# Optimization experiments

Hardware: AMD Instinct MI355X
Metric: run time of the kernel (lower is better)

The kernel has to match this reference:

```python
import jax, jax.numpy as jnp
import numpy as np
import math

H = 1024
E = 8
K = 2
CF = 1.5
THR = 0.5


def setup_inputs() -> dict:
    key = jax.random.key(0)
    ks = jax.random.split(key, 8)
    s = 0.02
    return {
        'hidden_states': jax.random.normal(ks[0], (2, 2048, H), jnp.float32),
        # importance predictor: Linear(H, H//2) -> ReLU -> Linear(H//2, 1) -> Sigmoid
        'wi1': jax.random.normal(ks[1], (H, H // 2), jnp.float32) * s,
        'bi1': jnp.zeros((H // 2,), jnp.float32),
        'wi2': jax.random.normal(ks[2], (H // 2, 1), jnp.float32) * s,
        'bi2': jnp.zeros((1,), jnp.float32),
        # router_important: Linear(H,H) -> ReLU -> Linear(H,E)
        'wr1': jax.random.normal(ks[3], (H, H), jnp.float32) * s,
        'br1': jnp.zeros((H,), jnp.float32),
        'wr2': jax.random.normal(ks[4], (H, E), jnp.float32) * s,
        'br2': jnp.zeros((E,), jnp.float32),
        # router_unimportant: Linear(H,H) -> ReLU -> Linear(H,E)
        'wu1': jax.random.normal(ks[5], (H, H), jnp.float32) * s,
        'bu1': jnp.zeros((H,), jnp.float32),
        'wu2': jax.random.normal(ks[6], (H, E), jnp.float32) * s,
        'bu2': jnp.zeros((E,), jnp.float32),
    }


def reference(hidden_states, wi1, bi1, wi2, bi2, wr1, br1, wr2, br2, wu1, bu1, wu2, bu2):
    x = hidden_states
    B, S, _ = x.shape
    N = B * S
    capacity = int(B * S * CF * K / E)  # static per-expert capacity

    # dual-gate routing
    importance = jax.nn.sigmoid(jnp.maximum(x @ wi1 + bi1, 0.0) @ wi2 + bi2)  # [B,S,1]
    imp_mask = (importance > THR).astype(x.dtype)                              # [B,S,1]
    logits_imp = jnp.maximum(x @ wr1 + br1, 0.0) @ wr2 + br2                   # [B,S,E]
    logits_unimp = jnp.maximum(x @ wu1 + bu1, 0.0) @ wu2 + bu2                 # [B,S,E]
    router_logits = imp_mask * logits_imp + (1.0 - imp_mask) * logits_unimp
    router_probs = jax.nn.softmax(router_logits, axis=-1)                      # [B,S,E]

    top_k_probs, top_k_indices = jax.lax.top_k(router_probs, K)
    top_k_probs = top_k_probs / top_k_probs.sum(-1, keepdims=True)

    # capacity-constrained dispatch: k-major assignment order (outer loop over k,
    # tokens in order), position within expert = running count, drop if >= capacity
    ef = top_k_indices.reshape(N, K).T.reshape(-1)   # [K*N] expert id, k-major
    pf = top_k_probs.reshape(N, K).T.reshape(-1)     # [K*N] gate prob
    tf = jnp.tile(jnp.arange(N), K)                  # [K*N] token id
    oh = jax.nn.one_hot(ef, E, dtype=jnp.int32)      # [K*N, E]
    pos = jnp.take_along_axis(jnp.cumsum(oh, axis=0), ef[:, None], 1)[:, 0] - 1
    keep = pos < capacity
    posc = jnp.clip(pos, 0, capacity - 1)

    zeros = jnp.zeros((N, E, capacity), x.dtype)
    dispatch = zeros.at[tf, ef, posc].add(keep.astype(x.dtype))
    combine = zeros.at[tf, ef, posc].add(jnp.where(keep, pf, 0.0))
    dispatch = dispatch.reshape(B, S, E, capacity)
    combine = combine.reshape(B, S, E, capacity)

    # aux losses
    rppe = router_probs.mean((0, 1))
    entropy_loss = jnp.sum(rppe * jnp.log(rppe * E + 1e-9))
    imp_sum = (router_probs * imp_mask).sum((0, 1)) + 1e-9
    ippe = imp_sum / imp_sum.sum()
    imp_entropy = -jnp.sum(ippe * jnp.log(ippe + 1e-9))
    aux_loss = entropy_loss - 0.1 * (imp_entropy / math.log(E))

    return dispatch, combine, router_probs, aux_loss, importance
```

## Files before the change

### kernel.cpp

```cpp
#include <hip/hip_runtime.h>
#include <math.h>

#define HDIM  1024
#define HHALF 512
#define NEXP  8
#define NTOK  4096
#define CAP   1536
#define NTOT  2560
#define TOTAL_DC (2u * NTOK * NEXP * CAP)

typedef _Float16 f16x8 __attribute__((ext_vector_type(8)));
typedef float    f32x4 __attribute__((ext_vector_type(4)));

#define GEMM_BLOCKS 640
#define FILL_BLOCKS 1408
#define S_LO 2048.0f
#define S_W  32.0f

__global__ __launch_bounds__(256) void prep(
    const float* __restrict__ x,
    const float* __restrict__ wi1, const float* __restrict__ wr1,
    const float* __restrict__ wu1,
    const float* __restrict__ bi1, const float* __restrict__ br1,
    const float* __restrict__ bu1,
    _Float16* __restrict__ Ah, _Float16* __restrict__ Al,
    _Float16* __restrict__ Bth, _Float16* __restrict__ Btl,
    float* __restrict__ bias_cat)
{
    __shared__ float tile[64][65];
    const int bid = blockIdx.x, tid = threadIdx.x;

    if (bid < 2048) {
        const int i8 = bid * 256 + tid;
        const float4* x4 = (const float4*)x;
        float4 v0 = x4[i8 * 2];
        float4 v1 = x4[i8 * 2 + 1];
        float f[8] = {v0.x, v0.y, v0.z, v0.w, v1.x, v1.y, v1.z, v1.w};
        f16x8 hi, lo;
#pragma unroll
        for (int j = 0; j < 8; j++) {
            _Float16 h = (_Float16)f[j];
            hi[j] = h;
            lo[j] = (_Float16)((f[j] - (float)h) * S_LO);
        }
        *(f16x8*)&Ah[(size_t)i8 * 8] = hi;
        *(f16x8*)&Al[(size_t)i8 * 8] = lo;
        return;
    }
    if (bid < 2688) {
        int local; const float* src; int C, nof;
        int b = bid - 2048;
        if (b < 128)      { src = wi1; C = 512;  nof = 0;    local = b; }
        else if (b < 384) { src = wr1; C = 1024; nof = 512;  local = b - 128; }
        else              { src = wu1; C = 1024; nof = 1536; local = b - 384; }
        const int nti = local >> 4, kti = local & 15;
#pragma unroll
        for (int p = 0; p < 16; p++) {
            int e = p * 256 + tid;
            int kr = e >> 6, nc = e & 63;
            tile[kr][nc] = src[(size_t)(kti * 64 + kr) * C + nti * 64 + nc];
        }
        __syncthreads();
#pragma unroll
        for (int p = 0; p < 16; p++) {
            int e = p * 256 + tid;
            int nl = e >> 6, kk = e & 63;
            float w32 = tile[kk][nl] * S_W;
            _Float16 h = (_Float16)w32;
            _Float16 l = (_Float16)((w32 - (float)h) * S_LO);
            const size_t o = (size_t)(nof + nti * 64 + nl) * 1024 + kti * 64 + kk;
            Bth[o] = h;
            Btl[o] = l;
        }
        return;
    }
    for (int i = tid; i < NTOT; i += 256) {
        float v = (i < 512) ? bi1[i] : (i < 1536) ? br1[i - 512] : bu1[i - 1536];
        bias_cat[i] = v;
    }
}

__global__ __launch_bounds__(256, 2) void gemm_fill(
    const _Float16* __restrict__ Ah, const _Float16* __restrict__ Al,
    const _Float16* __restrict__ Bth, const _Float16* __restrict__ Btl,
    const float* __restrict__ bias_cat, float* __restrict__ H,
    float* __restrict__ out)
{
    if (blockIdx.x >= GEMM_BLOCKS) {
        f32x4* o4 = (f32x4*)out;
        const unsigned total4 = TOTAL_DC / 4;
        unsigned i = (blockIdx.x - GEMM_BLOCKS) * 256u + threadIdx.x;
        const unsigned stride = FILL_BLOCKS * 256u;
        const f32x4 z = {0.f, 0.f, 0.f, 0.f};
        for (; i < total4; i += stride)
            __builtin_nontemporal_store(z, o4 + i);
        return;
    }

    __shared__ _Float16 lds[2][4][128][32];

    const int tid = threadIdx.x;
    const int lane = tid & 63, wid = tid >> 6;

    const int xcd = blockIdx.x & 7;
    const int idx = blockIdx.x >> 3;
    const int bm  = xcd * 4 + (idx & 3);
    const int bn  = idx >> 2;
    const int rowBase = bm * 128, colBase = bn * 128;

    const _Float16* gb =
        (wid == 0) ? Ah  + (size_t)rowBase * 1024 :
        (wid == 1) ? Al  + (size_t)rowBase * 1024 :
        (wid == 2) ? Bth + (size_t)colBase * 1024 :
                     Btl + (size_t)colBase * 1024;
    const int lrow = lane >> 2;
    const int lkg  = lane & 3;

    f32x4 acc_hh[4][4], acc_x[4][4];
    const f32x4 z4 = {0.f, 0.f, 0.f, 0.f};
#pragma unroll
    for (int i = 0; i < 4; i++)
#pragma unroll
        for (int j = 0; j < 4; j++) { acc_hh[i][j] = z4; acc_x[i][j] = z4; }

    const int mw = (wid >> 1) * 64, nw = (wid & 1) * 64;
    const int fr = lane & 15, s = lane >> 4;

#define STAGE(buf, k0)                                                        \
    {                                                                         \
        _Pragma("unroll")                                                     \
        for (int i = 0; i < 8; i++) {                                         \
            const int r = i * 16 + lrow;                                      \
            __builtin_amdgcn_global_load_lds(                                 \
                (const void*)(gb + (size_t)r * 1024 + (k0) + lkg * 8),        \
                (void*)&lds[buf][wid][i * 16][0], 16, 0, 0);                  \
        }                                                                     \
    }

#define COMPUTE(buf)                                                          \
    {                                                                         \
        f16x8 fa_h[4], fa_l[4], fb_h[4], fb_l[4];                             \
        _Pragma("unroll")                                                     \
        for (int mf = 0; mf < 4; mf++) {                                      \
            fa_h[mf] = *(const f16x8*)&lds[buf][0][mw + mf * 16 + fr][s * 8]; \
            fa_l[mf] = *(const f16x8*)&lds[buf][1][mw + mf * 16 + fr][s * 8]; \
        }                                                                     \
        _Pragma("unroll")                                                     \
        for (int nf = 0; nf < 4; nf++) {                                      \
            fb_h[nf] = *(const f16x8*)&lds[buf][2][nw + nf * 16 + fr][s * 8]; \
            fb_l[nf] = *(const f16x8*)&lds[buf][3][nw + nf * 16 + fr][s * 8]; \
        }                                                                     \
        _Pragma("unroll")                                                     \
        for (int mf = 0; mf < 4; mf++)                                        \
            _Pragma("unroll")                                                 \
            for (int nf = 0; nf < 4; nf++) {                                  \
                acc_hh[mf][nf] = __builtin_amdgcn_mfma_f32_16x16x32_f16(      \
                    fa_h[mf], fb_h[nf], acc_hh[mf][nf], 0, 0, 0);             \
                acc_x[mf][nf] = __builtin_amdgcn_mfma_f32_16x16x32_f16(       \
                    fa_h[mf], fb_l[nf], acc_x[mf][nf], 0, 0, 0);              \
                acc_x[mf][nf] = __builtin_amdgcn_mfma_f32_16x16x32_f16(       \
                    fa_l[mf], fb_h[nf], acc_x[mf][nf], 0, 0, 0);              \
            }                                                                 \
    }

    STAGE(0, 0);
    __syncthreads();

    for (int t = 0; t < 32; t += 2) {
        if (t + 1 < 32) STAGE(1, (t + 1) * 32);
        COMPUTE(0);
        __syncthreads();
        if (t + 2 < 32) STAGE(0, (t + 2) * 32);
        COMPUTE(1);
        __syncthreads();
    }
#undef STAGE
#undef COMPUTE

#pragma unroll
    for (int mf = 0; mf < 4; mf++) {
        const int row0 = rowBase + mw + mf * 16 + (lane >> 4) * 4;
#pragma unroll
        for (int nf = 0; nf < 4; nf++) {
            const int col = colBase + nw + nf * 16 + (lane & 15);
            const float b = bias_cat[col];
#pragma unroll
            for (int r = 0; r < 4; r++) {
                float v = (acc_hh[mf][nf][r] + acc_x[mf][nf][r] * (1.0f / S_LO))
                          * (1.0f / S_W) + b;
                H[(size_t)(row0 + r) * NTOT + col] = fmaxf(v, 0.f);
            }
        }
    }
}

__global__ __launch_bounds__(256) void second_layer(
    const float* __restrict__ H,
    const float* __restrict__ wi2, const float* __restrict__ bi2,
    const float* __restrict__ wr2, const float* __restrict__ br2,
    const float* __restrict__ wu2, const float* __restrict__ bu2,
    float* __restrict__ oprobs, float* __restrict__ oimp,
    int* __restrict__ tke, float* __restrict__ tkp)
{
    const int t = blockIdx.x;
    const int tid = threadIdx.x;
    const float* hrow = H + (size_t)t * NTOT;

    float pi = 0.f;
    float pr[8], pu[8];
#pragma unroll
    for (int e = 0; e < 8; e++) { pr[e] = 0.f; pu[e] = 0.f; }

    for (int j = tid; j < HHALF; j += 256) pi = fmaf(hrow[j], wi2[j], pi);
    for (int j = tid; j < HDIM; j += 256) {
        float a = hrow[512 + j], b = hrow[1536 + j];
#pragma unroll
        for (int e = 0; e < 8; e++) {
            pr[e] = fmaf(a, wr2[j * 8 + e], pr[e]);
            pu[e] = fmaf(b, wu2[j * 8 + e], pu[e]);
        }
    }

#pragma unroll
    for (int off = 32; off > 0; off >>= 1) {
        pi += __shfl_down(pi, off, 64);
#pragma unroll
        for (int e = 0; e < 8; e++) {
            pr[e] += __shfl_down(pr[e], off, 64);
            pu[e] += __shfl_down(pu[e], off, 64);
        }
    }

    __shared__ float red[4][17];
    const int lane = tid & 63, wv = tid >> 6;
    if (lane == 0) {
        red[wv][0] = pi;
#pragma unroll
        for (int e = 0; e < 8; e++) { red[wv][1 + e] = pr[e]; red[wv][9 + e] = pu[e]; }
    }
    __syncthreads();

    if (tid == 0) {
        float si = red[0][0] + red[1][0] + red[2][0] + red[3][0] + bi2[0];
        float sig = 1.f / (1.f + expf(-si));
        oimp[t] = sig;
        const bool m = sig > 0.5f;
        float lg[8];
#pragma unroll
        for (int e = 0; e < 8; e++) {
            float vr = red[0][1 + e] + red[1][1 + e] + red[2][1 + e] + red[3][1 + e] + br2[e];
            float vu = red[0][9 + e] + red[1][9 + e] + red[2][9 + e] + red[3][9 + e] + bu2[e];
            lg[e] = m ? vr : vu;
        }
        float mx = lg[0];
#pragma unroll
        for (int e = 1; e < 8; e++) mx = fmaxf(mx, lg[e]);
        float p[8], sum = 0.f;
#pragma unroll
        for (int e = 0; e < 8; e++) { p[e] = expf(lg[e] - mx); sum += p[e]; }
        const float inv = 1.f / sum;
#pragma unroll
        for (int e = 0; e < 8; e++) { p[e] *= inv; oprobs[t * 8 + e] = p[e]; }
        int i1 = 0;
#pragma unroll
        for (int e = 1; e < 8; e++) if (p[e] > p[i1]) i1 = e;
        int i2 = (i1 == 0) ? 1 : 0;
#pragma unroll
        for (int e = 0; e < 8; e++) if (e != i1 && p[e] > p[i2]) i2 = e;
        const float ps = p[i1] + p[i2];
        tke[t]        = i1;
        tke[NTOK + t] = i2;
        tkp[t]        = p[i1] / ps;
        tkp[NTOK + t] = p[i2] / ps;
    }
}

__global__ __launch_bounds__(256) void aux_kernel(
    const float* __restrict__ oprobs, const float* __restrict__ oimp,
    float* __restrict__ oaux)
{
    const int tid = threadIdx.x;
    float ap[8], ai[8];
#pragma unroll
    for (int e = 0; e < 8; e++) { ap[e] = 0.f; ai[e] = 0.f; }

    for (int t = tid; t < NTOK; t += 256) {
        const float msk = (oimp[t] > 0.5f) ? 1.f : 0.f;
#pragma unroll
        for (int e = 0; e < 8; e++) {
            float p = oprobs[t * 8 + e];
            ap[e] += p;
            ai[e] = fmaf(msk, p, ai[e]);
        }
    }
#pragma unroll
    for (int off = 32; off > 0; off >>= 1) {
#pragma unroll
        for (int e = 0; e < 8; e++) {
            ap[e] += __shfl_down(ap[e], off, 64);
            ai[e] += __shfl_down(ai[e], off, 64);
        }
    }
    __shared__ float red[4][16];
    const int lane = tid & 63, wv = tid >> 6;
    if (lane == 0) {
#pragma unroll
        for (int e = 0; e < 8; e++) { red[wv][e] = ap[e]; red[wv][8 + e] = ai[e]; }
    }
    __syncthreads();
    if (tid == 0) {
        float ent = 0.f, tot = 0.f, isv[8];
#pragma unroll
        for (int e = 0; e < 8; e++) {
            float sp = red[0][e] + red[1][e] + red[2][e] + red[3][e];
            float sm = red[0][8 + e] + red[1][8 + e] + red[2][8 + e] + red[3][8 + e];
            float r = sp / (float)NTOK;
            ent += r * logf(r * 8.f + 1e-9f);
            isv[e] = sm + 1e-9f;
            tot += isv[e];
        }
        float ie = 0.f;
#pragma unroll
        for (int e = 0; e < 8; e++) {
            float q = isv[e] / tot;
            ie -= q * logf(q + 1e-9f);
        }
        oaux[0] = ent - 0.1f * (ie / logf(8.f));
    }
}

__global__ __launch_bounds__(256) void scan_scatter(
    const int* __restrict__ tke, const float* __restrict__ tkp,
    float* __restrict__ out)
{
    __shared__ unsigned char se[2 * NTOK];
    __shared__ float         sp[2 * NTOK];
    __shared__ int cnts[256][8];

    const int tid = threadIdx.x;

    for (int i = tid; i < 2 * NTOK; i += 256) {
        se[i] = (unsigned char)tke[i];
        sp[i] = tkp[i];
    }
    __syncthreads();

    const int base = tid * 32;
    int c[8];
#pragma unroll
    for (int e = 0; e < 8; e++) c[e] = 0;
    for (int i = 0; i < 32; i++) {
        int e = se[base + i];
#pragma unroll
        for (int k = 0; k < 8; k++) c[k] += (e == k) ? 1 : 0;
    }
#pragma unroll
    for (int e = 0; e < 8; e++) cnts[tid][e] = c[e];
    __syncthreads();

    if (tid < 8) {
        int run = 0;
        for (int i = 0; i < 256; i++) {
            int v = cnts[i][tid];
            cnts[i][tid] = run;
            run += v;
        }
    }
    __syncthreads();

    int basecnt[8];
#pragma unroll
    for (int e = 0; e < 8; e++) basecnt[e] = cnts[tid][e];

    float* comb = out + (size_t)NTOK * NEXP * CAP;

    for (int i = 0; i < 32; i++) {
        const int idx = base + i;
        const int e = se[idx];
        int pos = 0;
#pragma unroll
        for (int k = 0; k < 8; k++)
            if (e == k) { pos = basecnt[k]; basecnt[k]++; }
        if (pos < CAP) {
            const int tok = idx & (NTOK - 1);
            const size_t o = ((size_t)tok * NEXP + e) * CAP + pos;
            out[o]  = 1.0f;
            comb[o] = sp[idx];
        }
    }
}

__global__ __launch_bounds__(256) void gemm_bias_relu(
    const float* __restrict__ A, const float* __restrict__ B,
    const float* __restrict__ bias, float* __restrict__ Hout, int N)
{
    __shared__ float As[16][132];
    __shared__ float Bs[16][132];
    const int tid = threadIdx.x;
    const int tx = tid & 15, ty = tid >> 4;
    const int rowBase = blockIdx.y * 128, colBase = blockIdx.x * 128;
    const int lrow = tid >> 1, lkq = (tid & 1) * 8;
    const int bkk = tid >> 4, bcol = (tid & 15) * 8;
    float acc[8][8];
#pragma unroll
    for (int i = 0; i < 8; i++)
#pragma unroll
        for (int j = 0; j < 8; j++) acc[i][j] = 0.f;
    const float* Aptr = A + (size_t)(rowBase + lrow) * HDIM + lkq;
    const float* Bptr = B + (size_t)bkk * N + colBase + bcol;
    for (int k0 = 0; k0 < HDIM; k0 += 16) {
        float4 a0 = *(const float4*)(Aptr + k0);
        float4 a1 = *(const float4*)(Aptr + k0 + 4);
        float4 b0 = *(const float4*)(Bptr + (size_t)k0 * N);
        float4 b1 = *(const float4*)(Bptr + (size_t)k0 * N + 4);
        __syncthreads();
        As[lkq + 0][lrow] = a0.x; As[lkq + 1][lrow] = a0.y;
        As[lkq + 2][lrow] = a0.z; As[lkq + 3][lrow] = a0.w;
        As[lkq + 4][lrow] = a1.x; As[lkq + 5][lrow] = a1.y;
        As[lkq + 6][lrow] = a1.z; As[lkq + 7][lrow] = a1.w;
        *(float4*)&Bs[bkk][bcol] = b0;
        *(float4*)&Bs[bkk][bcol + 4] = b1;
        __syncthreads();
#pragma unroll
        for (int kk = 0; kk < 16; kk++) {
            float4 x0 = *(const float4*)&As[kk][ty * 8];
            float4 x1 = *(const float4*)&As[kk][ty * 8 + 4];
            float4 y0 = *(const float4*)&Bs[kk][tx * 8];
            float4 y1 = *(const float4*)&Bs[kk][tx * 8 + 4];
            float av[8] = {x0.x, x0.y, x0.z, x0.w, x1.x, x1.y, x1.z, x1.w};
            float bv[8] = {y0.x, y0.y, y0.z, y0.w, y1.x, y1.y, y1.z, y1.w};
#pragma unroll
            for (int i = 0; i < 8; i++)
#pragma unroll
                for (int j = 0; j < 8; j++)
                    acc[i][j] = fmaf(av[i], bv[j], acc[i][j]);
        }
    }
#pragma unroll
    for (int i = 0; i < 8; i++) {
        const int r = rowBase + ty * 8 + i, c = colBase + tx * 8;
#pragma unroll
        for (int j = 0; j < 8; j += 4) {
            float4 v;
            v.x = fmaxf(acc[i][j + 0] + bias[c + j + 0], 0.f);
            v.y = fmaxf(acc[i][j + 1] + bias[c + j + 1], 0.f);
            v.z = fmaxf(acc[i][j + 2] + bias[c + j + 2], 0.f);
            v.w = fmaxf(acc[i][j + 3] + bias[c + j + 3], 0.f);
            *(float4*)&Hout[(size_t)r * N + c + j] = v;
        }
    }
}

__global__ __launch_bounds__(256) void zerofill_fb(float* __restrict__ out)
{
    f32x4* o4 = (f32x4*)out;
    const unsigned total4 = TOTAL_DC / 4;
    unsigned i = blockIdx.x * 256u + threadIdx.x;
    const unsigned stride = gridDim.x * 256u;
    const f32x4 z = {0.f, 0.f, 0.f, 0.f};
    for (; i < total4; i += stride) o4[i] = z;
}

__global__ __launch_bounds__(256) void second_layer_sep(
    const float* __restrict__ h_i, const float* __restrict__ h_r,
    const float* __restrict__ h_u,
    const float* __restrict__ wi2, const float* __restrict__ bi2,
    const float* __restrict__ wr2, const float* __restrict__ br2,
    const float* __restrict__ wu2, const float* __restrict__ bu2,
    float* __restrict__ oprobs, float* __restrict__ oimp,
    int* __restrict__ tke, float* __restrict__ tkp)
{
    const int t = blockIdx.x;
    const int tid = threadIdx.x;
    float pi = 0.f;
    float pr[8], pu[8];
#pragma unroll
    for (int e = 0; e < 8; e++) { pr[e] = 0.f; pu[e] = 0.f; }
    const float* hi = h_i + (size_t)t * HHALF;
    const float* hr = h_r + (size_t)t * HDIM;
    const float* hu = h_u + (size_t)t * HDIM;
    for (int j = tid; j < HHALF; j += 256) pi = fmaf(hi[j], wi2[j], pi);
    for (int j = tid; j < HDIM; j += 256) {
        float a = hr[j], b = hu[j];
#pragma unroll
        for (int e = 0; e < 8; e++) {
            pr[e] = fmaf(a, wr2[j * 8 + e], pr[e]);
            pu[e] = fmaf(b, wu2[j * 8 + e], pu[e]);
        }
    }
#pragma unroll
    for (int off = 32; off > 0; off >>= 1) {
        pi += __shfl_down(pi, off, 64);
#pragma unroll
        for (int e = 0; e < 8; e++) {
            pr[e] += __shfl_down(pr[e], off, 64);
            pu[e] += __shfl_down(pu[e], off, 64);
        }
    }
    __shared__ float red[4][17];
    const int lane = tid & 63, wv = tid >> 6;
    if (lane == 0) {
        red[wv][0] = pi;
#pragma unroll
        for (int e = 0; e < 8; e++) { red[wv][1 + e] = pr[e]; red[wv][9 + e] = pu[e]; }
    }
    __syncthreads();
    if (tid == 0) {
        float si = red[0][0] + red[1][0] + red[2][0] + red[3][0] + bi2[0];
        float sig = 1.f / (1.f + expf(-si));
        oimp[t] = sig;
        const bool m = sig > 0.5f;
        float lg[8];
#pragma unroll
        for (int e = 0; e < 8; e++) {
            float vr = red[0][1 + e] + red[1][1 + e] + red[2][1 + e] + red[3][1 + e] + br2[e];
            float vu = red[0][9 + e] + red[1][9 + e] + red[2][9 + e] + red[3][9 + e] + bu2[e];
            lg[e] = m ? vr : vu;
        }
        float mx = lg[0];
#pragma unroll
        for (int e = 1; e < 8; e++) mx = fmaxf(mx, lg[e]);
        float p[8], s = 0.f;
#pragma unroll
        for (int e = 0; e < 8; e++) { p[e] = expf(lg[e] - mx); s += p[e]; }
        const float inv = 1.f / s;
#pragma unroll
        for (int e = 0; e < 8; e++) { p[e] *= inv; oprobs[t * 8 + e] = p[e]; }
        int i1 = 0;
#pragma unroll
        for (int e = 1; e < 8; e++) if (p[e] > p[i1]) i1 = e;
        int i2 = (i1 == 0) ? 1 : 0;
#pragma unroll
        for (int e = 0; e < 8; e++) if (e != i1 && p[e] > p[i2]) i2 = e;
        const float ps = p[i1] + p[i2];
        tke[t]        = i1;
        tke[NTOK + t] = i2;
        tkp[t]        = p[i1] / ps;
        tkp[NTOK + t] = p[i2] / ps;
    }
}

extern "C" void kernel_launch(void* const* d_in, const int* in_sizes, int n_in,
                              void* d_out, int out_size, void* d_ws, size_t ws_size,
                              hipStream_t stream) {
    const float* x   = (const float*)d_in[0];
    const float* wi1 = (const float*)d_in[1];
    const float* bi1 = (const float*)d_in[2];
    const float* wi2 = (const float*)d_in[3];
    const float* bi2 = (const float*)d_in[4];
    const float* wr1 = (const float*)d_in[5];
    const float* br1 = (const float*)d_in[6];
    const float* wr2 = (const float*)d_in[7];
    const float* br2 = (const float*)d_in[8];
    const float* wu1 = (const float*)d_in[9];
    const float* bu1 = (const float*)d_in[10];
    const float* wu2 = (const float*)d_in[11];
    const float* bu2 = (const float*)d_in[12];

    float* out    = (float*)d_out;
    float* oprobs = out + (size_t)TOTAL_DC;
    float* oaux   = oprobs + NTOK * NEXP;
    float* oimp   = oaux + 1;

    const size_t szH  = (size_t)NTOK * NTOT * 4;
    const size_t szA  = (size_t)NTOK * HDIM * 2;
    const size_t szB  = (size_t)NTOT * HDIM * 2;
    const size_t need = szH + 2 * szA + 2 * szB + NTOT * 4
                      + 2 * NTOK * 4 + 2 * NTOK * 4 + 4096;
    dim3 blk(256);

    if (ws_size >= need) {
        char* p = (char*)d_ws;
        float*    H    = (float*)p;            p += szH;
        _Float16* Ah   = (_Float16*)p;         p += szA;
        _Float16* Al   = (_Float16*)p;         p += szA;
        _Float16* Bth  = (_Float16*)p;         p += szB;
        _Float16* Btl  = (_Float16*)p;         p += szB;
        float*    bias = (float*)p;            p += NTOT * 4;
        int*      tke  = (int*)p;              p += 2 * NTOK * 4;
        float*    tkp  = (float*)p;

        prep<<<2689, blk, 0, stream>>>(x, wi1, wr1, wu1, bi1, br1, bu1,
                                       Ah, Al, Bth, Btl, bias);
        gemm_fill<<<GEMM_BLOCKS + FILL_BLOCKS, blk, 0, stream>>>(
            Ah, Al, Bth, Btl, bias, H, out);
        second_layer<<<NTOK, blk, 0, stream>>>(H, wi2, bi2, wr2, br2, wu2, bu2,
                                               oprobs, oimp, tke, tkp);
        aux_kernel<<<1, blk, 0, stream>>>(oprobs, oimp, oaux);
        scan_scatter<<<1, blk, 0, stream>>>(tke, tkp, out);
    } else {
        float* h_i = out;
        float* h_r = h_i + (size_t)NTOK * HHALF;
        float* h_u = h_r + (size_t)NTOK * HDIM;
        int*   tke  = (int*)d_ws;
        float* tkp  = (float*)d_ws + 2 * NTOK;

        gemm_bias_relu<<<dim3(HHALF / 128, NTOK / 128), blk, 0, stream>>>(x, wi1, bi1, h_i, HHALF);
        gemm_bias_relu<<<dim3(HDIM / 128, NTOK / 128), blk, 0, stream>>>(x, wr1, br1, h_r, HDIM);
        gemm_bias_relu<<<dim3(HDIM / 128, NTOK / 128), blk, 0, stream>>>(x, wu1, bu1, h_u, HDIM);
        second_layer_sep<<<NTOK, blk, 0, stream>>>(h_i, h_r, h_u, wi2, bi2, wr2, br2,
                                                   wu2, bu2, oprobs, oimp, tke, tkp);
        aux_kernel<<<1, blk, 0, stream>>>(oprobs, oimp, oaux);
        zerofill_fb<<<2048, blk, 0, stream>>>(out);
        scan_scatter<<<1, blk, 0, stream>>>(tke, tkp, out);
    }
}
```

Baseline: 179.0 us.

## Fuse second-layer projections into GEMM epilogue and merge aux with scan

The GEMM epilogue now applies bias and ReLU, multiplies by the second-layer weights in registers, and writes per-column-tile partial logits. This removes the full hidden-activation matrix round trip through HBM. A new per-thread reduce_route kernel sums the partials and performs sigmoid, softmax and top-2. The aux-loss kernel is merged into the single-block scan/scatter kernel. Block indices are interleaved so GEMM and zero-fill blocks are spread across XCDs, at the cost of a larger epilogue with more registers and shuffles.

```diff
diff --git a/kernel.cpp b/kernel.cpp
--- a/kernel.cpp
+++ b/kernel.cpp
@@ -12,8 +12,8 @@
 typedef _Float16 f16x8 __attribute__((ext_vector_type(8)));
 typedef float    f32x4 __attribute__((ext_vector_type(4)));
 
-#define GEMM_BLOCKS 640
-#define FILL_BLOCKS 1408
+#define TOTAL_BLOCKS 2048
+#define FILL_BLOCKS  1408
 #define S_LO 2048.0f
 #define S_W  32.0f
 
@@ -83,13 +83,20 @@
 __global__ __launch_bounds__(256, 2) void gemm_fill(
     const _Float16* __restrict__ Ah, const _Float16* __restrict__ Al,
     const _Float16* __restrict__ Bth, const _Float16* __restrict__ Btl,
-    const float* __restrict__ bias_cat, float* __restrict__ H,
-    float* __restrict__ out)
+    const float* __restrict__ bias_cat,
+    const float* __restrict__ wi2, const float* __restrict__ wr2,
+    const float* __restrict__ wu2,
+    float* __restrict__ part, float* __restrict__ out)
 {
-    if (blockIdx.x >= GEMM_BLOCKS) {
+    const int octet = blockIdx.x >> 3;
+    const int sub   = blockIdx.x & 7;
+    const int om    = octet & 15;
+
+    if (om >= 5) {
+        const int fo = (octet >> 4) * 11 + (om - 5);
         f32x4* o4 = (f32x4*)out;
         const unsigned total4 = TOTAL_DC / 4;
-        unsigned i = (blockIdx.x - GEMM_BLOCKS) * 256u + threadIdx.x;
+        unsigned i = (unsigned)(fo * 8 + sub) * 256u + threadIdx.x;
         const unsigned stride = FILL_BLOCKS * 256u;
         const f32x4 z = {0.f, 0.f, 0.f, 0.f};
         for (; i < total4; i += stride)
@@ -102,8 +109,9 @@
     const int tid = threadIdx.x;
     const int lane = tid & 63, wid = tid >> 6;
 
-    const int xcd = blockIdx.x & 7;
-    const int idx = blockIdx.x >> 3;
+    const int g   = ((octet >> 4) * 5 + om) * 8 + sub;
+    const int xcd = g & 7;
+    const int idx = g >> 3;
     const int bm  = xcd * 4 + (idx & 3);
     const int bn  = idx >> 2;
     const int rowBase = bm * 128, colBase = bn * 128;
@@ -177,113 +185,148 @@
 #undef STAGE
 #undef COMPUTE
 
+    const int seg = (bn < 4) ? 0 : (bn < 12 ? 1 : 2);
+    const int half = wid & 1;
+    float w2v[4][8];
+    float bcol[4];
+#pragma unroll
+    for (int nf = 0; nf < 4; nf++) {
+        const int c = colBase + nw + nf * 16 + fr;
+        bcol[nf] = bias_cat[c];
+        if (seg == 0) {
+            w2v[nf][0] = wi2[c];
+        } else if (seg == 1) {
+            const float4* w4 = (const float4*)&wr2[(c - 512) * 8];
+            float4 a = w4[0], b = w4[1];
+            w2v[nf][0] = a.x; w2v[nf][1] = a.y; w2v[nf][2] = a.z; w2v[nf][3] = a.w;
+            w2v[nf][4] = b.x; w2v[nf][5] = b.y; w2v[nf][6] = b.z; w2v[nf][7] = b.w;
+        } else {
+            const float4* w4 = (const float4*)&wu2[(c - 1536) * 8];
+            float4 a = w4[0], b = w4[1];
+            w2v[nf][0] = a.x; w2v[nf][1] = a.y; w2v[nf][2] = a.z; w2v[nf][3] = a.w;
+            w2v[nf][4] = b.x; w2v[nf][5] = b.y; w2v[nf][6] = b.z; w2v[nf][7] = b.w;
+        }
+    }
+
+    const int tgroup = lane >> 4;
 #pragma unroll
     for (int mf = 0; mf < 4; mf++) {
-        const int row0 = rowBase + mw + mf * 16 + (lane >> 4) * 4;
-#pragma unroll
-        for (int nf = 0; nf < 4; nf++) {
-            const int col = colBase + nw + nf * 16 + (lane & 15);
-            const float b = bias_cat[col];
-#pragma unroll
-            for (int r = 0; r < 4; r++) {
+        const int tok0 = rowBase + mw + mf * 16 + tgroup * 4;
+#pragma unroll
+        for (int r = 0; r < 4; r++) {
+            float sacc[8];
+#pragma unroll
+            for (int e = 0; e < 8; e++) sacc[e] = 0.f;
+#pragma unroll
+            for (int nf = 0; nf < 4; nf++) {
                 float v = (acc_hh[mf][nf][r] + acc_x[mf][nf][r] * (1.0f / S_LO))
-                          * (1.0f / S_W) + b;
-                H[(size_t)(row0 + r) * NTOT + col] = fmaxf(v, 0.f);
+                          * (1.0f / S_W) + bcol[nf];
+                v = fmaxf(v, 0.f);
+                if (seg == 0) {
+                    sacc[0] = fmaf(v, w2v[nf][0], sacc[0]);
+                } else {
+#pragma unroll
+                    for (int e = 0; e < 8; e++)
+                        sacc[e] = fmaf(v, w2v[nf][e], sacc[e]);
+                }
             }
-        }
-    }
-}
-
-__global__ __launch_bounds__(256) void second_layer(
-    const float* __restrict__ H,
-    const float* __restrict__ wi2, const float* __restrict__ bi2,
-    const float* __restrict__ wr2, const float* __restrict__ br2,
-    const float* __restrict__ wu2, const float* __restrict__ bu2,
+            const int nE = (seg == 0) ? 1 : 8;
+            for (int e = 0; e < nE; e++) {
+                float xv = sacc[e];
+                xv += __shfl_xor(xv, 1, 64);
+                xv += __shfl_xor(xv, 2, 64);
+                xv += __shfl_xor(xv, 4, 64);
+                xv += __shfl_xor(xv, 8, 64);
+                if (fr == 0)
+                    part[(((size_t)bn * 2 + half) * NTOK + (tok0 + r)) * 8 + e] = xv;
+            }
+        }
+    }
+}
+
+__global__ __launch_bounds__(256) void reduce_route(
+    const float* __restrict__ part,
+    const float* __restrict__ bi2, const float* __restrict__ br2,
+    const float* __restrict__ bu2,
     float* __restrict__ oprobs, float* __restrict__ oimp,
     int* __restrict__ tke, float* __restrict__ tkp)
 {
-    const int t = blockIdx.x;
+    const int t = blockIdx.x * 256 + threadIdx.x;
+
+    float imp = bi2[0];
+#pragma unroll
+    for (int sl = 0; sl < 8; sl++)
+        imp += part[((size_t)sl * NTOK + t) * 8];
+
+    float lr[8], lu[8];
+#pragma unroll
+    for (int e = 0; e < 8; e++) { lr[e] = br2[e]; lu[e] = bu2[e]; }
+#pragma unroll
+    for (int sl = 8; sl < 24; sl++) {
+        const float4* p4 = (const float4*)&part[((size_t)sl * NTOK + t) * 8];
+        float4 a = p4[0], b = p4[1];
+        lr[0] += a.x; lr[1] += a.y; lr[2] += a.z; lr[3] += a.w;
+        lr[4] += b.x; lr[5] += b.y; lr[6] += b.z; lr[7] += b.w;
+    }
+#pragma unroll
+    for (int sl = 24; sl < 40; sl++) {
+        const float4* p4 = (const float4*)&part[((size_t)sl * NTOK + t) * 8];
+        float4 a = p4[0], b = p4[1];
+        lu[0] += a.x; lu[1] += a.y; lu[2] += a.z; lu[3] += a.w;
+        lu[4] += b.x; lu[5] += b.y; lu[6] += b.z; lu[7] += b.w;
+    }
+
+    const float sig = 1.f / (1.f + expf(-imp));
+    oimp[t] = sig;
+    const bool m = sig > 0.5f;
+    float lg[8];
+#pragma unroll
+    for (int e = 0; e < 8; e++) lg[e] = m ? lr[e] : lu[e];
+
+    float mx = lg[0];
+#pragma unroll
+    for (int e = 1; e < 8; e++) mx = fmaxf(mx, lg[e]);
+    float p[8], sum = 0.f;
+#pragma unroll
+    for (int e = 0; e < 8; e++) { p[e] = expf(lg[e] - mx); sum += p[e]; }
+    const float inv = 1.f / sum;
+#pragma unroll
+    for (int e = 0; e < 8; e++) { p[e] *= inv; oprobs[t * 8 + e] = p[e]; }
+
+    int i1 = 0;
+#pragma unroll
+    for (int e = 1; e < 8; e++) if (p[e] > p[i1]) i1 = e;
+    int i2 = (i1 == 0) ? 1 : 0;
+#pragma unroll
+    for (int e = 0; e < 8; e++) if (e != i1 && p[e] > p[i2]) i2 = e;
+    const float ps = p[i1] + p[i2];
+    tke[t]        = i1;
+    tke[NTOK + t] = i2;
+    tkp[t]        = p[i1] / ps;
+    tkp[NTOK + t] = p[i2] / ps;
+}
+
+__global__ __launch_bounds__(256) void scan_scatter_aux(
+    const int* __restrict__ tke, const float* __restrict__ tkp,
+    const float* __restrict__ oprobs, const float* __restrict__ oimp,
+    float* __restrict__ out, float* __restrict__ oaux)
+{
+    __shared__ unsigned char se[2 * NTOK];
+    __shared__ float         sp[2 * NTOK];
+    __shared__ int  cnts[256][8];
+    __shared__ float red[4][16];
+
     const int tid = threadIdx.x;
-    const float* hrow = H + (size_t)t * NTOT;
-
-    float pi = 0.f;
-    float pr[8], pu[8];
-#pragma unroll
-    for (int e = 0; e < 8; e++) { pr[e] = 0.f; pu[e] = 0.f; }
-
-    for (int j = tid; j < HHALF; j += 256) pi = fmaf(hrow[j], wi2[j], pi);
-    for (int j = tid; j < HDIM; j += 256) {
-        float a = hrow[512 + j], b = hrow[1536 + j];
-#pragma unroll
-        for (int e = 0; e < 8; e++) {
-            pr[e] = fmaf(a, wr2[j * 8 + e], pr[e]);
-            pu[e] = fmaf(b, wu2[j * 8 + e], pu[e]);
-        }
-    }
-
-#pragma unroll
-    for (int off = 32; off > 0; off >>= 1) {
-        pi += __shfl_down(pi, off, 64);
-#pragma unroll
-        for (int e = 0; e < 8; e++) {
-            pr[e] += __shfl_down(pr[e], off, 64);
-            pu[e] += __shfl_down(pu[e], off, 64);
-        }
-    }
-
-    __shared__ float red[4][17];
     const int lane = tid & 63, wv = tid >> 6;
-    if (lane == 0) {
-        red[wv][0] = pi;
-#pragma unroll
-        for (int e = 0; e < 8; e++) { red[wv][1 + e] = pr[e]; red[wv][9 + e] = pu[e]; }
-    }
-    __syncthreads();
-
-    if (tid == 0) {
-        float si = red[0][0] + red[1][0] + red[2][0] + red[3][0] + bi2[0];
-        float sig = 1.f / (1.f + expf(-si));
-        oimp[t] = sig;
-        const bool m = sig > 0.5f;
-        float lg[8];
-#pragma unroll
-        for (int e = 0; e < 8; e++) {
-            float vr = red[0][1 + e] + red[1][1 + e] + red[2][1 + e] + red[3][1 + e] + br2[e];
-            float vu = red[0][9 + e] + red[1][9 + e] + red[2][9 + e] + red[3][9 + e] + bu2[e];
-            lg[e] = m ? vr : vu;
-        }
-        float mx = lg[0];
-#pragma unroll
-        for (int e = 1; e < 8; e++) mx = fmaxf(mx, lg[e]);
-        float p[8], sum = 0.f;
-#pragma unroll
-        for (int e = 0; e < 8; e++) { p[e] = expf(lg[e] - mx); sum += p[e]; }
-        const float inv = 1.f / sum;
-#pragma unroll
-        for (int e = 0; e < 8; e++) { p[e] *= inv; oprobs[t * 8 + e] = p[e]; }
-        int i1 = 0;
-#pragma unroll
-        for (int e = 1; e < 8; e++) if (p[e] > p[i1]) i1 = e;
-        int i2 = (i1 == 0) ? 1 : 0;
-#pragma unroll
-        for (int e = 0; e < 8; e++) if (e != i1 && p[e] > p[i2]) i2 = e;
-        const float ps = p[i1] + p[i2];
-        tke[t]        = i1;
-        tke[NTOK + t] = i2;
-        tkp[t]        = p[i1] / ps;
-        tkp[NTOK + t] = p[i2] / ps;
-    }
-}
-
-__global__ __launch_bounds__(256) void aux_kernel(
-    const float* __restrict__ oprobs, const float* __restrict__ oimp,
-    float* __restrict__ oaux)
-{
-    const int tid = threadIdx.x;
+
+    for (int i = tid; i < 2 * NTOK; i += 256) {
+        se[i] = (unsigned char)tke[i];
+        sp[i] = tkp[i];
+    }
+
     float ap[8], ai[8];
 #pragma unroll
     for (int e = 0; e < 8; e++) { ap[e] = 0.f; ai[e] = 0.f; }
-
     for (int t = tid; t < NTOK; t += 256) {
         const float msk = (oimp[t] > 0.5f) ? 1.f : 0.f;
 #pragma unroll
@@ -301,8 +344,6 @@
             ai[e] += __shfl_down(ai[e], off, 64);
         }
     }
-    __shared__ float red[4][16];
-    const int lane = tid & 63, wv = tid >> 6;
     if (lane == 0) {
 #pragma unroll
         for (int e = 0; e < 8; e++) { red[wv][e] = ap[e]; red[wv][8 + e] = ai[e]; }
@@ -312,9 +353,9 @@
         float ent = 0.f, tot = 0.f, isv[8];
 #pragma unroll
         for (int e = 0; e < 8; e++) {
-            float sp = red[0][e] + red[1][e] + red[2][e] + red[3][e];
-            float sm = red[0][8 + e] + red[1][8 + e] + red[2][8 + e] + red[3][8 + e];
-            float r = sp / (float)NTOK;
+            float spr = red[0][e] + red[1][e] + red[2][e] + red[3][e];
+            float sm  = red[0][8 + e] + red[1][8 + e] + red[2][8 + e] + red[3][8 + e];
+            float r = spr / (float)NTOK;
             ent += r * logf(r * 8.f + 1e-9f);
             isv[e] = sm + 1e-9f;
             tot += isv[e];
@@ -327,23 +368,6 @@
         }
         oaux[0] = ent - 0.1f * (ie / logf(8.f));
     }
-}
-
-__global__ __launch_bounds__(256) void scan_scatter(
-    const int* __restrict__ tke, const float* __restrict__ tkp,
-    float* __restrict__ out)
-{
-    __shared__ unsigned char se[2 * NTOK];
-    __shared__ float         sp[2 * NTOK];
-    __shared__ int cnts[256][8];
-
-    const int tid = threadIdx.x;
-
-    for (int i = tid; i < 2 * NTOK; i += 256) {
-        se[i] = (unsigned char)tke[i];
-        sp[i] = tkp[i];
-    }
-    __syncthreads();
 
     const int base = tid * 32;
     int c[8];
@@ -562,32 +586,31 @@
     float* oaux   = oprobs + NTOK * NEXP;
     float* oimp   = oaux + 1;
 
-    const size_t szH  = (size_t)NTOK * NTOT * 4;
     const size_t szA  = (size_t)NTOK * HDIM * 2;
     const size_t szB  = (size_t)NTOT * HDIM * 2;
-    const size_t need = szH + 2 * szA + 2 * szB + NTOT * 4
+    const size_t szP  = (size_t)40 * NTOK * 8 * 4;
+    const size_t need = 2 * szA + 2 * szB + NTOT * 4 + szP
                       + 2 * NTOK * 4 + 2 * NTOK * 4 + 4096;
     dim3 blk(256);
 
     if (ws_size >= need) {
         char* p = (char*)d_ws;
-        float*    H    = (float*)p;            p += szH;
         _Float16* Ah   = (_Float16*)p;         p += szA;
         _Float16* Al   = (_Float16*)p;         p += szA;
         _Float16* Bth  = (_Float16*)p;         p += szB;
         _Float16* Btl  = (_Float16*)p;         p += szB;
         float*    bias = (float*)p;            p += NTOT * 4;
+        float*    part = (float*)p;            p += szP;
         int*      tke  = (int*)p;              p += 2 * NTOK * 4;
         float*    tkp  = (float*)p;
 
         prep<<<2689, blk, 0, stream>>>(x, wi1, wr1, wu1, bi1, br1, bu1,
                                        Ah, Al, Bth, Btl, bias);
-        gemm_fill<<<GEMM_BLOCKS + FILL_BLOCKS, blk, 0, stream>>>(
-            Ah, Al, Bth, Btl, bias, H, out);
-        second_layer<<<NTOK, blk, 0, stream>>>(H, wi2, bi2, wr2, br2, wu2, bu2,
-                                               oprobs, oimp, tke, tkp);
-        aux_kernel<<<1, blk, 0, stream>>>(oprobs, oimp, oaux);
-        scan_scatter<<<1, blk, 0, stream>>>(tke, tkp, out);
+        gemm_fill<<<TOTAL_BLOCKS, blk, 0, stream>>>(
+            Ah, Al, Bth, Btl, bias, wi2, wr2, wu2, part, out);
+        reduce_route<<<NTOK / 256, blk, 0, stream>>>(
+            part, bi2, br2, bu2, oprobs, oimp, tke, tkp);
+        scan_scatter_aux<<<1, blk, 0, stream>>>(tke, tkp, oprobs, oimp, out, oaux);
     } else {
         float* h_i = out;
         float* h_r = h_i + (size_t)NTOK * HHALF;
@@ -600,8 +623,7 @@
         gemm_bias_relu<<<dim3(HDIM / 128, NTOK / 128), blk, 0, stream>>>(x, wu1, bu1, h_u, HDIM);
         second_layer_sep<<<NTOK, blk, 0, stream>>>(h_i, h_r, h_u, wi2, bi2, wr2, br2,
                                                    wu2, bu2, oprobs, oimp, tke, tkp);
-        aux_kernel<<<1, blk, 0, stream>>>(oprobs, oimp, oaux);
         zerofill_fb<<<2048, blk, 0, stream>>>(out);
-        scan_scatter<<<1, blk, 0, stream>>>(tke, tkp, out);
-    }
-}
+        scan_scatter_aux<<<1, blk, 0, stream>>>(tke, tkp, oprobs, oimp, out, oaux);
+    }
+}
```

Result: slower. 209.9 us (+17.3%).
